# Optimization experiments

Hardware: AMD Instinct MI355X
Metric: run time of the kernel (lower is better)

## Reference

```python
import jax, jax.numpy as jnp
import numpy as np

NC, NG, NP = 8192, 4096, 140
FD, D, L = 512, 256, 2
E_OBS, E_COEXP, E_PPI, E_SYM = 300000, 200000, 10000, 20000
EPS = 1e-5


def layer_norm(x, g, b):
    mu = jnp.mean(x, -1, keepdims=True)
    v = jnp.mean((x - mu) ** 2, -1, keepdims=True)
    return (x - mu) * jax.lax.rsqrt(v + EPS) * g + b


def sage(h_src, h_dst, src, dst, w, Ws, Wn, b, n_dst):
    # DGL SAGEConv (mean aggregator, edge-weighted): mean over incoming
    # weighted messages, then fc_self(h_dst) + fc_neigh(neigh) + bias.
    m = h_src[src] * w[:, None]                                  # [E, D]
    neigh = jax.ops.segment_sum(m, dst, num_segments=n_dst)      # [n_dst, D]
    deg = jax.ops.segment_sum(jnp.ones_like(w), dst, num_segments=n_dst)
    neigh = neigh / jnp.maximum(deg, 1.0)[:, None]
    return h_dst @ Ws + neigh @ Wn + b


def setup_inputs() -> dict:
    key = jax.random.key(0)
    ks = iter(jax.random.split(key, 64))
    def n(*s):
        return jax.random.normal(next(ks), s, jnp.float32) * 0.02
    def u(e):
        return jax.random.uniform(next(ks), (e,), jnp.float32)
    def ri(e, hi):
        return jax.random.randint(next(ks), (e,), 0, hi, jnp.int32)
    return dict(
        cell_feat=jax.random.normal(next(ks), (NC, FD), jnp.float32),
        gene_feat=jax.random.normal(next(ks), (NG, FD), jnp.float32),
        pro_idx=jnp.arange(NP, dtype=jnp.int32),
        obs_src=ri(E_OBS, NG), obs_dst=ri(E_OBS, NC), obs_w=u(E_OBS),
        rev_obs_src=ri(E_OBS, NC), rev_obs_dst=ri(E_OBS, NG), rev_obs_w=u(E_OBS),
        symbol_src=ri(E_SYM, NG), symbol_dst=ri(E_SYM, NP), symbol_w=u(E_SYM),
        rev_symbol_src=ri(E_SYM, NP), rev_symbol_dst=ri(E_SYM, NG), rev_symbol_w=u(E_SYM),
        coexp_src=ri(E_COEXP, NG), coexp_dst=ri(E_COEXP, NG), coexp_w=u(E_COEXP),
        ppi_src=ri(E_PPI, NP), ppi_dst=ri(E_PPI, NP), ppi_w=u(E_PPI),
        W_emb_cell=n(FD, D), b_emb_cell=jnp.zeros((D,), jnp.float32),
        W_emb_gene=n(FD, D), b_emb_gene=jnp.zeros((D,), jnp.float32),
        emb_pro=n(NP, D),
        W_mlpcell=n(L, D, D), b_mlpcell=jnp.zeros((L, D), jnp.float32),
        W_sage_self=n(L, 6, D, D), W_sage_neigh=n(L, 6, D, D),
        b_sage=jnp.zeros((L, 6, D), jnp.float32),
        ln1_g=jnp.ones((L, 3, D), jnp.float32), ln1_b=jnp.zeros((L, 3, D), jnp.float32),
        ln2_g=jnp.ones((L, 3, D), jnp.float32), ln2_b=jnp.zeros((L, 3, D), jnp.float32),
        W_last=n(3 * D, NP), b_last=jnp.zeros((NP,), jnp.float32),
    )


def reference(cell_feat, gene_feat, pro_idx,
              obs_src, obs_dst, obs_w,
              rev_obs_src, rev_obs_dst, rev_obs_w,
              symbol_src, symbol_dst, symbol_w,
              rev_symbol_src, rev_symbol_dst, rev_symbol_w,
              coexp_src, coexp_dst, coexp_w,
              ppi_src, ppi_dst, ppi_w,
              W_emb_cell, b_emb_cell, W_emb_gene, b_emb_gene, emb_pro,
              W_mlpcell, b_mlpcell, W_sage_self, W_sage_neigh, b_sage,
              ln1_g, ln1_b, ln2_g, ln2_b, W_last, b_last):
    act = jax.nn.selu
    hc = cell_feat @ W_emb_cell + b_emb_cell      # emb_cell
    hg = gene_feat @ W_emb_gene + b_emb_gene      # emb_gene
    hp = emb_pro[pro_idx]                         # nn.Embedding path
    nc, ng, npn = hc.shape[0], hg.shape[0], hp.shape[0]
    hist = [hc]
    for l in range(W_mlpcell.shape[0]):
        Ws, Wn, bs = W_sage_self[l], W_sage_neigh[l], b_sage[l]
        hmlp = layer_norm(act(hc @ W_mlpcell[l] + b_mlpcell[l]), ln1_g[l, 2], ln1_b[l, 2])
        # HeteroGraphConv(SAGE) over edges_sub = [obs, rev_obs, symbol, rev_symbol] (stack)
        s_obs = sage(hg, hc, obs_src, obs_dst, obs_w, Ws[0], Wn[0], bs[0], nc)
        s_robs = sage(hc, hg, rev_obs_src, rev_obs_dst, rev_obs_w, Ws[1], Wn[1], bs[1], ng)
        s_sym = sage(hg, hp, symbol_src, symbol_dst, symbol_w, Ws[2], Wn[2], bs[2], npn)
        s_rsym = sage(hp, hg, rev_symbol_src, rev_symbol_dst, rev_symbol_w, Ws[3], Wn[3], bs[3], ng)
        # homogeneous subgraph convs: gene_sage on coexp, pro_sage on ppi
        h_gg = layer_norm(act(sage(hg, hg, coexp_src, coexp_dst, coexp_w, Ws[4], Wn[4], bs[4], ng)), ln1_g[l, 0], ln1_b[l, 0])
        h_pp = layer_norm(act(sage(hp, hp, ppi_src, ppi_dst, ppi_w, Ws[5], Wn[5], bs[5], npn)), ln1_g[l, 1], ln1_b[l, 1])
        # norm each stacked relation output, then agg='sum' over the stack dim
        hgen = layer_norm(act(s_robs), ln1_g[l, 0], ln1_b[l, 0]) + layer_norm(act(s_rsym), ln1_g[l, 0], ln1_b[l, 0]) + h_gg
        hpro = layer_norm(act(s_sym), ln1_g[l, 1], ln1_b[l, 1]) + h_pp
        hcel = layer_norm(act(s_obs), ln1_g[l, 2], ln1_b[l, 2]) + hmlp
        hg = layer_norm(act(hgen), ln2_g[l, 0], ln2_b[l, 0])
        hp = layer_norm(act(hpro), ln2_g[l, 1], ln2_b[l, 1])
        hc = layer_norm(act(hcel), ln2_g[l, 2], ln2_b[l, 2])
        hist.append(hc)
    # mlp_last over concat of per-layer cell reps (sum(dims[1:-1]) -> dims[-1])
    return jnp.concatenate(hist, -1) @ W_last + b_last
```

## Files before the change

kernel.cpp:

```cpp
#include <hip/hip_runtime.h>

typedef unsigned short ushort_t;
typedef unsigned int uint_t;

typedef ushort_t ushortx8 __attribute__((ext_vector_type(8)));
typedef ushort_t ushortx4 __attribute__((ext_vector_type(4)));
typedef __bf16 bf16x8 __attribute__((ext_vector_type(8)));
typedef float f32x4 __attribute__((ext_vector_type(4)));

#define NCC 8192
#define NGG 4096
#define NPP 140
#define LDS_STR 88
#define CEPB 16384

__device__ __forceinline__ float bf2f(ushort_t u) {
    uint_t i = ((uint_t)u) << 16;
    float f;
    __builtin_memcpy(&f, &i, 4);
    return f;
}
__device__ __forceinline__ ushort_t f2bf(float f) {
    uint_t i;
    __builtin_memcpy(&i, &f, 4);
    uint_t r = (i + 0x7FFFu + ((i >> 16) & 1u)) >> 16;
    return (ushort_t)r;
}
__device__ __forceinline__ float scrub(float x) {
    return __builtin_isfinite(x) ? x : 0.f;
}
__device__ __forceinline__ float selu_f(float x) {
    return x > 0.f ? 1.0507009873554805f * x : 1.7580993408473766f * expm1f(x);
}
__device__ __forceinline__ float wsum64(float x) {
    for (int o = 32; o; o >>= 1) x += __shfl_xor(x, o, 64);
    return x;
}

__global__ __launch_bounds__(256) void sc_zero1(int* __restrict__ a, int na) {
    int i = blockIdx.x * 256 + threadIdx.x;
    if (i < na) a[i] = 0;
}

struct CountJob {
    const int* dst;
    const int* src;
    const float* w;
    uint_t* pw;
    ushort_t* rank;
    int E;
    int nbins;
    int* deg;
    int bstart;
};
struct CountBatch {
    CountJob j[6];
};
struct TrJob {
    const float* src;
    ushort_t* dst;
    int K, N, nx, nxy;
    int bstart;
};
struct TrBatch {
    TrJob j[6];
};
struct FillJob {
    const int* dst;
    const uint_t* pw;
    const ushort_t* rank;
    int E;
    const int* offs;
    uint_t* ep;
    int bstart;
};
struct FillBatch {
    FillJob j[6];
};
struct GemmJob {
    const void* A1;
    int lda1, K1, af1;
    const ushort_t* Bt1;
    const ushort_t* A2;
    int K2;
    const ushort_t* Bt2;
    const float* bias;
    ushort_t* C;
    int ldc, M;
    int mstart;
};
struct GemmBatch {
    GemmJob j[7];
};

struct CountArgs {
    CountBatch cb;
    int bsC;
    const float* cf;
    ushort_t* cf16;
    int nbC;
    int nbCvt;
    const float* gf;
    ushort_t* gf16;
    TrBatch tb;
    int bsT;
    const float* emb;
    const int* pidx;
    ushort_t* hp;
    int nEmb;
};
__global__ __launch_bounds__(1024) void sc_count(CountArgs ca) {
    __shared__ int hist[NCC];
    int bx = blockIdx.x;
    const int tid = threadIdx.x;
    if (bx >= ca.bsC) {
        bx -= ca.bsC;
        if (bx < ca.nbCvt) {
            const float* src;
            ushort_t* dst;
            if (bx < ca.nbC) {
                src = ca.cf;
                dst = ca.cf16;
            } else {
                bx -= ca.nbC;
                src = ca.gf;
                dst = ca.gf16;
            }
            size_t i = ((size_t)bx * 1024 + tid) * 8;
            float4 f0 = *(const float4*)(src + i);
            float4 f1 = *(const float4*)(src + i + 4);
            ushortx8 v;
            v[0] = f2bf(f0.x);
            v[1] = f2bf(f0.y);
            v[2] = f2bf(f0.z);
            v[3] = f2bf(f0.w);
            v[4] = f2bf(f1.x);
            v[5] = f2bf(f1.y);
            v[6] = f2bf(f1.z);
            v[7] = f2bf(f1.w);
            *(ushortx8*)(dst + i) = v;
            return;
        }
        bx -= ca.nbCvt;
        if (bx < ca.bsT) {
            ushort_t* tt = (ushort_t*)hist;
            int r = 0;
#pragma unroll
            for (int i = 1; i < 6; ++i) r = (bx >= ca.tb.j[i].bstart) ? i : r;
            const TrJob& J = ca.tb.j[r];
            int local = bx - J.bstart;
            int b = local / J.nxy, rem = local % J.nxy;
            int n0 = (rem % J.nx) * 32, k0 = (rem / J.nx) * 32;
            const float* s = J.src + (size_t)b * J.K * J.N;
            ushort_t* d = J.dst + (size_t)b * J.K * J.N;
            int x = tid & 31, y = tid >> 5;
            {
                int k = k0 + y, n = n0 + x;
                tt[y * 33 + x] = (k < J.K && n < J.N) ? f2bf(s[(size_t)k * J.N + n]) : (ushort_t)0;
            }
            __syncthreads();
            {
                int n = n0 + y, k = k0 + x;
                if (n < J.N && k < J.K) d[(size_t)n * J.K + k] = tt[x * 33 + y];
            }
            return;
        }
        bx -= ca.bsT;
        int i = bx * 1024 + tid;
        if (i < ca.nEmb) {
            int r = i >> 8, c = i & 255;
            int j = ca.pidx[r];
            j = (uint_t)j < (uint_t)NPP ? j : 0;
            ca.hp[i] = f2bf(ca.emb[(size_t)j * 256 + c]);
        }
        return;
    }
    int r = 0;
#pragma unroll
    for (int i = 1; i < 6; ++i) r = (bx >= ca.cb.j[i].bstart) ? i : r;
    const CountJob& J = ca.cb.j[r];
    const int nb = J.nbins;
    for (int b = tid; b < nb; b += 1024) hist[b] = 0;
    __syncthreads();
    const int e0 = (bx - J.bstart) * CEPB;
    ushort_t lrk[16];
#pragma unroll
    for (int u = 0; u < 16; ++u) {
        int e = e0 + u * 1024 + tid;
        if (e < J.E) {
            int d = J.dst[e];
            lrk[u] = (ushort_t)atomicAdd(&hist[d], 1);
            J.pw[e] = ((uint_t)f2bf(J.w[e]) << 16) | (uint_t)J.src[e];
        }
    }
    __syncthreads();
    for (int b = tid; b < nb; b += 1024) {
        int c = hist[b];
        if (c > 0) hist[b] = atomicAdd(&J.deg[b], c);
    }
    __syncthreads();
#pragma unroll
    for (int u = 0; u < 16; ++u) {
        int e = e0 + u * 1024 + tid;
        if (e < J.E) {
            int d = J.dst[e];
            J.rank[e] = (ushort_t)(hist[d] + (int)lrk[u]);
        }
    }
}

__global__ __launch_bounds__(1024) void sc_csr_scan6(const int* __restrict__ deg_base,
                                                     int* __restrict__ offs_base) {
    const int ndst[6] = {NCC, NGG, NPP, NGG, NGG, NPP};
    const int dstart[6] = {0, NCC, NCC + NGG, NCC + NGG + NPP, NCC + 2 * NGG + NPP,
                           NCC + 3 * NGG + NPP};
    const int ostart[6] = {0, NCC + 1, NCC + NGG + 2, NCC + NGG + NPP + 3,
                           NCC + 2 * NGG + NPP + 4, NCC + 3 * NGG + NPP + 5};
    int r = blockIdx.x;
    const int* deg = deg_base + dstart[r];
    int* offs = offs_base + ostart[r];
    int n = ndst[r];
    __shared__ int wsum[16];
    __shared__ int carry;
    int tid = threadIdx.x, wave = tid >> 6, lane = tid & 63;
    if (tid == 0) carry = 0;
    __syncthreads();
    for (int base = 0; base < n; base += 1024) {
        int i = base + tid;
        int v = (i < n) ? deg[i] : 0;
        int x = v;
#pragma unroll
        for (int o = 1; o < 64; o <<= 1) {
            int tv = __shfl_up(x, o, 64);
            if (lane >= o) x += tv;
        }
        if (lane == 63) wsum[wave] = x;
        __syncthreads();
        if (tid == 0) {
            int acc = 0;
#pragma unroll
            for (int k = 0; k < 16; ++k) {
                int tv = wsum[k];
                wsum[k] = acc;
                acc += tv;
            }
        }
        __syncthreads();
        int incl = x + wsum[wave];
        int cr = carry;
        if (i < n) offs[i] = cr + incl - v;
        __syncthreads();
        if (tid == 1023) carry = cr + incl;
        __syncthreads();
    }
    if (tid == 0) offs[n] = carry;
}

__device__ __forceinline__ void gemm_body(const GemmBatch& gbat, int mbx, int n0, ushort_t* As,
                                          ushort_t* Bs) {
    int r = 0;
#pragma unroll
    for (int i = 1; i < 7; ++i) r = (mbx >= gbat.j[i].mstart) ? i : r;
    const void* JA1 = gbat.j[r].A1;
    const int lda1 = gbat.j[r].lda1, K1j = gbat.j[r].K1, af1 = gbat.j[r].af1;
    const ushort_t* JBt1 = gbat.j[r].Bt1;
    const ushort_t* JA2 = gbat.j[r].A2;
    const int K2j = gbat.j[r].K2;
    const ushort_t* JBt2 = gbat.j[r].Bt2;
    const float* bias = gbat.j[r].bias;
    ushort_t* C = gbat.j[r].C;
    const int ldc = gbat.j[r].ldc, M = gbat.j[r].M;
    const int tid = threadIdx.x;
    const int wave = tid >> 6, lane = tid & 63;
    const int lr = lane & 15, lq = lane >> 4;
    const int m0 = (mbx - gbat.j[r].mstart) * 128;
    f32x4 acc[2][4] = {};
    for (int pass = 0; pass < 2; ++pass) {
        const void* A = pass ? (const void*)JA2 : JA1;
        const ushort_t* Bt = pass ? JBt2 : JBt1;
        const int K = pass ? K2j : K1j;
        const int lda = pass ? 256 : lda1;
        const int af = pass ? 0 : af1;
        if (K == 0 || A == nullptr) continue;
        for (int k0 = 0; k0 < K; k0 += 64) {
            __syncthreads();
#pragma unroll
            for (int i = 0; i < 4; ++i) {
                int g = tid + i * 256;
                int rr = g >> 3, c = (g & 7) * 8;
                ushortx8 v = {0, 0, 0, 0, 0, 0, 0, 0};
                int gm = m0 + rr;
                if (gm < M) {
                    if (af) {
                        const float* Af = (const float*)A;
                        float4 f0 = *(const float4*)(Af + (size_t)gm * lda + k0 + c);
                        float4 f1 = *(const float4*)(Af + (size_t)gm * lda + k0 + c + 4);
                        v[0] = f2bf(f0.x);
                        v[1] = f2bf(f0.y);
                        v[2] = f2bf(f0.z);
                        v[3] = f2bf(f0.w);
                        v[4] = f2bf(f1.x);
                        v[5] = f2bf(f1.y);
                        v[6] = f2bf(f1.z);
                        v[7] = f2bf(f1.w);
                    } else {
                        v = *(const ushortx8*)((const ushort_t*)A + (size_t)gm * lda + k0 + c);
                    }
                }
                *(ushortx8*)(&As[rr * LDS_STR + c]) = v;
            }
#pragma unroll
            for (int i = 0; i < 2; ++i) {
                int g = tid + i * 256;
                int rr = g >> 3, c = (g & 7) * 8;
                int gn = n0 + rr;
                ushortx8 v = *(const ushortx8*)(Bt + (size_t)gn * K + k0 + c);
                *(ushortx8*)(&Bs[rr * LDS_STR + c]) = v;
            }
            __syncthreads();
#pragma unroll
            for (int kk = 0; kk < 64; kk += 32) {
                bf16x8 a0 = __builtin_bit_cast(
                    bf16x8, *(const ushortx8*)(&As[(wave * 32 + lr) * LDS_STR + kk + lq * 8]));
                bf16x8 a1 = __builtin_bit_cast(
                    bf16x8,
                    *(const ushortx8*)(&As[(wave * 32 + 16 + lr) * LDS_STR + kk + lq * 8]));
                bf16x8 b0 = __builtin_bit_cast(
                    bf16x8, *(const ushortx8*)(&Bs[(lr)*LDS_STR + kk + lq * 8]));
                bf16x8 b1 = __builtin_bit_cast(
                    bf16x8, *(const ushortx8*)(&Bs[(16 + lr) * LDS_STR + kk + lq * 8]));
                bf16x8 b2 = __builtin_bit_cast(
                    bf16x8, *(const ushortx8*)(&Bs[(32 + lr) * LDS_STR + kk + lq * 8]));
                bf16x8 b3 = __builtin_bit_cast(
                    bf16x8, *(const ushortx8*)(&Bs[(48 + lr) * LDS_STR + kk + lq * 8]));
                acc[0][0] = __builtin_amdgcn_mfma_f32_16x16x32_bf16(a0, b0, acc[0][0], 0, 0, 0);
                acc[0][1] = __builtin_amdgcn_mfma_f32_16x16x32_bf16(a0, b1, acc[0][1], 0, 0, 0);
                acc[0][2] = __builtin_amdgcn_mfma_f32_16x16x32_bf16(a0, b2, acc[0][2], 0, 0, 0);
                acc[0][3] = __builtin_amdgcn_mfma_f32_16x16x32_bf16(a0, b3, acc[0][3], 0, 0, 0);
                acc[1][0] = __builtin_amdgcn_mfma_f32_16x16x32_bf16(a1, b0, acc[1][0], 0, 0, 0);
                acc[1][1] = __builtin_amdgcn_mfma_f32_16x16x32_bf16(a1, b1, acc[1][1], 0, 0, 0);
                acc[1][2] = __builtin_amdgcn_mfma_f32_16x16x32_bf16(a1, b2, acc[1][2], 0, 0, 0);
                acc[1][3] = __builtin_amdgcn_mfma_f32_16x16x32_bf16(a1, b3, acc[1][3], 0, 0, 0);
            }
        }
    }
#pragma unroll
    for (int mt = 0; mt < 2; ++mt)
#pragma unroll
        for (int nt = 0; nt < 4; ++nt) {
            int col = n0 + nt * 16 + lr;
            float bb = bias[col];
#pragma unroll
            for (int v = 0; v < 4; ++v) {
                int row = m0 + wave * 32 + mt * 16 + lq * 4 + v;
                if (row >= M) continue;
                C[(size_t)row * ldc + col] = f2bf(scrub(acc[mt][nt][v] + bb));
            }
        }
}

__global__ __launch_bounds__(256) void sc_gemm_batch(GemmBatch gbat) {
    __shared__ __align__(16) ushort_t As[128 * LDS_STR];
    __shared__ __align__(16) ushort_t Bs[64 * LDS_STR];
    gemm_body(gbat, blockIdx.x, blockIdx.y * 64, As, Bs);
}

struct Emb64Job {
    const ushort_t* A;
    const ushort_t* Bt;
    const float* bias;
    ushort_t* C;
    int ldc;
    ushort_t* C2;
    int mstart;
};
struct FillGemmArgs {
    Emb64Job ej[2];
    int gemmBlocks;
    FillBatch fb;
};
__global__ __launch_bounds__(256) void sc_fill_gemm(FillGemmArgs fg) {
    __shared__ __align__(16) ushort_t As[64 * LDS_STR];
    __shared__ __align__(16) ushort_t Bs[64 * LDS_STR];
    int bx = blockIdx.x;
    if (bx >= fg.gemmBlocks) {
        bx -= fg.gemmBlocks;
        int r = 0;
#pragma unroll
        for (int i = 1; i < 6; ++i) r = (bx >= fg.fb.j[i].bstart) ? i : r;
        const FillJob& J = fg.fb.j[r];
        int e = (bx - J.bstart) * 256 + threadIdx.x;
        if (e < J.E) {
            int d = J.dst[e];
            J.ep[J.offs[d] + (int)J.rank[e]] = J.pw[e];
        }
        return;
    }
    const int mb = bx >> 2, n0 = (bx & 3) * 64;
    const int r = (mb >= fg.ej[1].mstart) ? 1 : 0;
    const Emb64Job& J = fg.ej[r];
    const int m0 = (mb - J.mstart) * 64;
    const ushort_t* A = J.A;
    const ushort_t* Bt = J.Bt;
    const int tid = threadIdx.x;
    const int wave = tid >> 6, lane = tid & 63;
    const int lr = lane & 15, lq = lane >> 4;
    f32x4 acc[4] = {};
    for (int k0 = 0; k0 < 512; k0 += 64) {
        __syncthreads();
#pragma unroll
        for (int i = 0; i < 2; ++i) {
            int g = tid + i * 256;
            int rr = g >> 3, c = (g & 7) * 8;
            *(ushortx8*)(&As[rr * LDS_STR + c]) =
                *(const ushortx8*)(A + (size_t)(m0 + rr) * 512 + k0 + c);
            *(ushortx8*)(&Bs[rr * LDS_STR + c]) =
                *(const ushortx8*)(Bt + (size_t)(n0 + rr) * 512 + k0 + c);
        }
        __syncthreads();
#pragma unroll
        for (int kk = 0; kk < 64; kk += 32) {
            bf16x8 a = __builtin_bit_cast(
                bf16x8, *(const ushortx8*)(&As[(wave * 16 + lr) * LDS_STR + kk + lq * 8]));
            bf16x8 b0 =
                __builtin_bit_cast(bf16x8, *(const ushortx8*)(&Bs[(lr)*LDS_STR + kk + lq * 8]));
            bf16x8 b1 = __builtin_bit_cast(
                bf16x8, *(const ushortx8*)(&Bs[(16 + lr) * LDS_STR + kk + lq * 8]));
            bf16x8 b2 = __builtin_bit_cast(
                bf16x8, *(const ushortx8*)(&Bs[(32 + lr) * LDS_STR + kk + lq * 8]));
            bf16x8 b3 = __builtin_bit_cast(
                bf16x8, *(const ushortx8*)(&Bs[(48 + lr) * LDS_STR + kk + lq * 8]));
            acc[0] = __builtin_amdgcn_mfma_f32_16x16x32_bf16(a, b0, acc[0], 0, 0, 0);
            acc[1] = __builtin_amdgcn_mfma_f32_16x16x32_bf16(a, b1, acc[1], 0, 0, 0);
            acc[2] = __builtin_amdgcn_mfma_f32_16x16x32_bf16(a, b2, acc[2], 0, 0, 0);
            acc[3] = __builtin_amdgcn_mfma_f32_16x16x32_bf16(a, b3, acc[3], 0, 0, 0);
        }
    }
#pragma unroll
    for (int nt = 0; nt < 4; ++nt) {
        int col = n0 + nt * 16 + lr;
        float bb = J.bias[col];
#pragma unroll
        for (int v = 0; v < 4; ++v) {
            int row = m0 + wave * 16 + lq * 4 + v;
            ushort_t val = f2bf(scrub(acc[nt][v] + bb));
            J.C[(size_t)row * J.ldc + col] = val;
            if (J.C2) J.C2[(size_t)row * 256 + col] = val;
// ... 38 lines not shown
                *(ushortx8*)(&As[rr * LDS_STR + c]) =
                    *(const ushortx8*)(ga.mA + (size_t)(m0 + rr) * 768 + k0 + c);
                *(ushortx8*)(&Bs[rr * LDS_STR + c]) =
                    *(const ushortx8*)(ga.mBt + (size_t)(n0 + rr) * 256 + k0 + c);
            }
            __syncthreads();
#pragma unroll
            for (int kk = 0; kk < 64; kk += 32) {
                bf16x8 a = __builtin_bit_cast(
                    bf16x8, *(const ushortx8*)(&As[(wave * 16 + lr) * LDS_STR + kk + lq * 8]));
                bf16x8 b0 = __builtin_bit_cast(
                    bf16x8, *(const ushortx8*)(&Bs[(lr)*LDS_STR + kk + lq * 8]));
                bf16x8 b1 = __builtin_bit_cast(
                    bf16x8, *(const ushortx8*)(&Bs[(16 + lr) * LDS_STR + kk + lq * 8]));
                bf16x8 b2 = __builtin_bit_cast(
                    bf16x8, *(const ushortx8*)(&Bs[(32 + lr) * LDS_STR + kk + lq * 8]));
                bf16x8 b3 = __builtin_bit_cast(
                    bf16x8, *(const ushortx8*)(&Bs[(48 + lr) * LDS_STR + kk + lq * 8]));
                acc[0] = __builtin_amdgcn_mfma_f32_16x16x32_bf16(a, b0, acc[0], 0, 0, 0);
                acc[1] = __builtin_amdgcn_mfma_f32_16x16x32_bf16(a, b1, acc[1], 0, 0, 0);
                acc[2] = __builtin_amdgcn_mfma_f32_16x16x32_bf16(a, b2, acc[2], 0, 0, 0);
                acc[3] = __builtin_amdgcn_mfma_f32_16x16x32_bf16(a, b3, acc[3], 0, 0, 0);
            }
        }
#pragma unroll
        for (int nt = 0; nt < 4; ++nt) {
            int col = n0 + nt * 16 + lr;
            float bb = ga.mbias[col];
#pragma unroll
            for (int v = 0; v < 4; ++v) {
                int row = m0 + wave * 16 + lq * 4 + v;
                ga.mC[(size_t)row * 256 + col] = f2bf(scrub(acc[nt][v] + bb));
            }
        }
        return;
    }
    bx -= ga.gemmBlocks;
    int grow = bx * 4 + (tid >> 6);
    if (grow >= ga.total_rows) return;
    int r = 0;
#pragma unroll
    for (int i = 1; i < 6; ++i) r = (grow >= ga.j[i].row_start) ? i : r;
    r = __builtin_amdgcn_readfirstlane(r);
    const char* hsrc = (const char*)ga.j[r].hsrc;
    const uint_t row_bytes = (uint_t)(ga.j[r].src_ld * 2);
    const uint_t src_n = (uint_t)ga.j[r].src_n;
    const int* offs = ga.j[r].offs;
    const uint_t* ep = ga.j[r].ep;
    ushort_t* out = ga.j[r].out;
    int row = grow - ga.j[r].row_start;
    int lane = tid & 63;
    int cb = lane * 8;
    int s0 = offs[row], s1 = offs[row + 1];
    float a0 = 0.f, a1 = 0.f, a2 = 0.f, a3 = 0.f;
    for (int base = s0; base < s1; base += 64) {
        int e = base + lane;
        uint_t myp = (e < s1) ? ep[e] : 0u;
        int cnt = s1 - base;
        cnt = cnt < 64 ? cnt : 64;
        int cnt16 = (cnt + 15) & ~15;
        for (int jj = 0; jj < cnt16; jj += 16) {
#pragma unroll
            for (int u = 0; u < 16; ++u) {
                uint_t pw = (uint_t)__builtin_amdgcn_readlane((int)myp, jj + u);
                uint_t s = pw & 0xFFFFu;
                s = s < src_n ? s : 0u;
                float w = bf2f((ushort_t)(pw >> 16));
                const uint2 v = *(const uint2*)(hsrc + (size_t)(s * row_bytes) + cb);
                uint_t x0 = v.x << 16, x1 = v.x & 0xFFFF0000u;
                uint_t x2 = v.y << 16, x3 = v.y & 0xFFFF0000u;
                a0 = fmaf(w, __builtin_bit_cast(float, x0), a0);
                a1 = fmaf(w, __builtin_bit_cast(float, x1), a1);
                a2 = fmaf(w, __builtin_bit_cast(float, x2), a2);
                a3 = fmaf(w, __builtin_bit_cast(float, x3), a3);
            }
        }
    }
    float inv = 1.f / fmaxf((float)(s1 - s0), 1.f);
    ushort_t* o = out + (size_t)row * 256 + lane * 4;
    o[0] = f2bf(scrub(a0 * inv));
    o[1] = f2bf(scrub(a1 * inv));
    o[2] = f2bf(scrub(a2 * inv));
    o[3] = f2bf(scrub(a3 * inv));
}

__global__ __launch_bounds__(256) void sc_gemm(const ushort_t* __restrict__ A1, int lda1,
                                               const ushort_t* __restrict__ Bt1, int K1,
                                               const float* __restrict__ bias,
                                               float* __restrict__ Cf, int ldc, int M, int N) {
    __shared__ __align__(16) ushort_t As[128 * LDS_STR];
    __shared__ __align__(16) ushort_t Bs[64 * LDS_STR];
    const int tid = threadIdx.x;
    const int wave = tid >> 6, lane = tid & 63;
    const int lr = lane & 15, lq = lane >> 4;
    const int m0 = blockIdx.x * 128, n0 = blockIdx.y * 64;
    f32x4 acc[2][4] = {};
    for (int k0 = 0; k0 < K1; k0 += 64) {
        __syncthreads();
#pragma unroll
        for (int i = 0; i < 4; ++i) {
            int g = tid + i * 256;
            int r = g >> 3, c = (g & 7) * 8;
            ushortx8 v = {0, 0, 0, 0, 0, 0, 0, 0};
            int gm = m0 + r;
            if (gm < M) v = *(const ushortx8*)(A1 + (size_t)gm * lda1 + k0 + c);
            *(ushortx8*)(&As[r * LDS_STR + c]) = v;
        }
#pragma unroll
        for (int i = 0; i < 2; ++i) {
            int g = tid + i * 256;
            int r = g >> 3, c = (g & 7) * 8;
            ushortx8 v = {0, 0, 0, 0, 0, 0, 0, 0};
            int gn = n0 + r;
            if (gn < N) v = *(const ushortx8*)(Bt1 + (size_t)gn * K1 + k0 + c);
            *(ushortx8*)(&Bs[r * LDS_STR + c]) = v;
        }
        __syncthreads();
#pragma unroll
        for (int kk = 0; kk < 64; kk += 32) {
            bf16x8 a0 = __builtin_bit_cast(
                bf16x8, *(const ushortx8*)(&As[(wave * 32 + lr) * LDS_STR + kk + lq * 8]));
            bf16x8 a1 = __builtin_bit_cast(
                bf16x8, *(const ushortx8*)(&As[(wave * 32 + 16 + lr) * LDS_STR + kk + lq * 8]));
            bf16x8 b0 =
                __builtin_bit_cast(bf16x8, *(const ushortx8*)(&Bs[(lr)*LDS_STR + kk + lq * 8]));
            bf16x8 b1 = __builtin_bit_cast(
                bf16x8, *(const ushortx8*)(&Bs[(16 + lr) * LDS_STR + kk + lq * 8]));
            bf16x8 b2 = __builtin_bit_cast(
                bf16x8, *(const ushortx8*)(&Bs[(32 + lr) * LDS_STR + kk + lq * 8]));
            bf16x8 b3 = __builtin_bit_cast(
                bf16x8, *(const ushortx8*)(&Bs[(48 + lr) * LDS_STR + kk + lq * 8]));
            acc[0][0] = __builtin_amdgcn_mfma_f32_16x16x32_bf16(a0, b0, acc[0][0], 0, 0, 0);
            acc[0][1] = __builtin_amdgcn_mfma_f32_16x16x32_bf16(a0, b1, acc[0][1], 0, 0, 0);
            acc[0][2] = __builtin_amdgcn_mfma_f32_16x16x32_bf16(a0, b2, acc[0][2], 0, 0, 0);
            acc[0][3] = __builtin_amdgcn_mfma_f32_16x16x32_bf16(a0, b3, acc[0][3], 0, 0, 0);
            acc[1][0] = __builtin_amdgcn_mfma_f32_16x16x32_bf16(a1, b0, acc[1][0], 0, 0, 0);
            acc[1][1] = __builtin_amdgcn_mfma_f32_16x16x32_bf16(a1, b1, acc[1][1], 0, 0, 0);
            acc[1][2] = __builtin_amdgcn_mfma_f32_16x16x32_bf16(a1, b2, acc[1][2], 0, 0, 0);
            acc[1][3] = __builtin_amdgcn_mfma_f32_16x16x32_bf16(a1, b3, acc[1][3], 0, 0, 0);
        }
    }
#pragma unroll
    for (int mt = 0; mt < 2; ++mt)
#pragma unroll
        for (int nt = 0; nt < 4; ++nt) {
            int col = n0 + nt * 16 + lr;
            if (col >= N) continue;
            float bb = bias ? bias[col] : 0.f;
#pragma unroll
            for (int v = 0; v < 4; ++v) {
                int row = m0 + wave * 32 + mt * 16 + lq * 4 + v;
                if (row >= M) continue;
                Cf[(size_t)row * ldc + col] = scrub(acc[mt][nt][v] + bb);
            }
        }
}

struct LnJob {
    const ushort_t *sA, *sB, *sC;
    const float *g1, *b1, *g2, *b2;
    ushort_t* out;
    int out_ld;
    ushort_t* out2;
    int row_start;
};
struct LnBatch {
// ... 83 lines not shown
    const float* b_sage = (const float*)d_in[30];
    const float* ln1_g = (const float*)d_in[31];
    const float* ln1_b = (const float*)d_in[32];
    const float* ln2_g = (const float*)d_in[33];
    const float* ln2_b = (const float*)d_in[34];
    const float* W_last = (const float*)d_in[35];
    const float* b_last = (const float*)d_in[36];

    const int E_obs = in_sizes[3], E_sym = in_sizes[9], E_coexp = in_sizes[15],
              E_ppi = in_sizes[18];
    const int Er[6] = {E_obs, E_obs, E_sym, E_sym, E_coexp, E_ppi};
    const int Nd[6] = {NCC, NGG, NPP, NGG, NGG, NPP};

    char* p = (char*)d_ws;
    auto carve = [&](size_t bytes) -> char* {
        char* r = p;
        p += ((bytes + 255) & ~(size_t)255);
        return r;
    };
    ushort_t* hist = (ushort_t*)carve((size_t)NCC * 768 * 2);
    ushort_t* hg = (ushort_t*)carve((size_t)NGG * 256 * 2);
    ushort_t* hp = (ushort_t*)carve((size_t)NPP * 256 * 2);
    ushort_t* n_obs = (ushort_t*)carve((size_t)NCC * 256 * 2);
    ushort_t* n_robs = (ushort_t*)carve((size_t)NGG * 256 * 2);
    ushort_t* n_sym = (ushort_t*)carve((size_t)NPP * 256 * 2);
    ushort_t* n_rsym = (ushort_t*)carve((size_t)NGG * 256 * 2);
    ushort_t* n_coexp = (ushort_t*)carve((size_t)NGG * 256 * 2);
    ushort_t* n_ppi = (ushort_t*)carve((size_t)NPP * 256 * 2);
    ushort_t* s_obs = (ushort_t*)carve((size_t)NCC * 256 * 2);
    ushort_t* s_robs = (ushort_t*)carve((size_t)NGG * 256 * 2);
    ushort_t* s_sym = (ushort_t*)carve((size_t)NPP * 256 * 2);
    ushort_t* s_rsym = (ushort_t*)carve((size_t)NGG * 256 * 2);
    ushort_t* s_coexp = (ushort_t*)carve((size_t)NGG * 256 * 2);
    ushort_t* s_ppi = (ushort_t*)carve((size_t)NPP * 256 * 2);
    ushort_t* s_mlp = (ushort_t*)carve((size_t)NCC * 256 * 2);
    ushort_t* Wt_emb_cell = (ushort_t*)carve((size_t)512 * 256 * 2);
    ushort_t* Wt_emb_gene = (ushort_t*)carve((size_t)512 * 256 * 2);
    ushort_t* Wt_mlp = (ushort_t*)carve((size_t)2 * 256 * 256 * 2);
    ushort_t* Wt_self = (ushort_t*)carve((size_t)12 * 256 * 256 * 2);
    ushort_t* Wt_neigh = (ushort_t*)carve((size_t)12 * 256 * 256 * 2);
    ushort_t* Wt_last = (ushort_t*)carve((size_t)140 * 768 * 2);
    const int NDTOT = NCC + 3 * NGG + 2 * NPP;
    int* deg_all = (int*)carve((size_t)NDTOT * 4);
    int* offs_all = (int*)carve((size_t)(NDTOT + 6) * 4);
    const int ETOT = 2 * E_obs + 2 * E_sym + E_coexp + E_ppi;
    uint_t* pw_all = (uint_t*)carve((size_t)ETOT * 4);
    ushort_t* rank_all = (ushort_t*)carve((size_t)ETOT * 2);
    uint_t* ep_all = (uint_t*)carve((size_t)ETOT * 4);
    ushort_t* hc_cmp = (ushort_t*)carve((size_t)NCC * 256 * 2);
    ushort_t* cf16 = s_obs;
    ushort_t* gf16 = s_coexp;
    (void)ws_size;
    (void)n_in;
    (void)out_size;

    const int dS[6] = {0, NCC, NCC + NGG, NCC + NGG + NPP, NCC + 2 * NGG + NPP,
                       NCC + 3 * NGG + NPP};
    const int oS[6] = {0, NCC + 1, NCC + NGG + 2, NCC + NGG + NPP + 3, NCC + 2 * NGG + NPP + 4,
                       NCC + 3 * NGG + NPP + 5};
    int eS[6];
    eS[0] = 0;
    eS[1] = eS[0] + E_obs;
    eS[2] = eS[1] + E_obs;
    eS[3] = eS[2] + E_sym;
    eS[4] = eS[3] + E_sym;
    eS[5] = eS[4] + E_coexp;

    sc_zero1<<<cdivi(NDTOT, 256), 256, 0, stream>>>(deg_all, NDTOT);
    {
        CountArgs ca;
        int bs = 0;
        for (int r = 0; r < 6; ++r) {
            ca.cb.j[r] = {edge_dst[r], edge_src[r], edge_w[r], pw_all + eS[r], rank_all + eS[r],
                          Er[r],       Nd[r],       deg_all + dS[r], bs};
            bs += cdivi(Er[r], CEPB);
        }
        ca.bsC = bs;
        ca.cf = cell_feat;
        ca.cf16 = cf16;
        ca.nbC = (NCC * 512) / 8192;
        ca.gf = gene_feat;
        ca.gf16 = gf16;
        int nbG = (NGG * 512) / 8192;
        ca.nbCvt = ca.nbC + nbG;
        int bt = 0;
        auto add = [&](int idx, const float* s, ushort_t* d, int B, int K, int N) {
            int nx = cdivi(N, 32), ny = cdivi(K, 32);
            ca.tb.j[idx] = {s, d, K, N, nx, nx * ny, bt};
            bt += B * nx * ny;
        };
        add(0, W_emb_cell, Wt_emb_cell, 1, 512, 256);
        add(1, W_emb_gene, Wt_emb_gene, 1, 512, 256);
        add(2, W_mlpcell, Wt_mlp, 2, 256, 256);
        add(3, W_sage_self, Wt_self, 12, 256, 256);
        add(4, W_sage_neigh, Wt_neigh, 12, 256, 256);
        add(5, W_last, Wt_last, 1, 768, 140);
        ca.bsT = bt;
        ca.emb = emb_pro;
        ca.pidx = pro_idx;
        ca.hp = hp;
        ca.nEmb = NPP * 256;
        int bsE = cdivi(NPP * 256, 1024);
        sc_count<<<bs + ca.nbCvt + bt + bsE, 1024, 0, stream>>>(ca);
    }
    sc_csr_scan6<<<6, 1024, 0, stream>>>(deg_all, offs_all);
    {
        FillGemmArgs fg;
        fg.ej[0] = {cf16, Wt_emb_cell, b_emb_cell, hist, 768, hc_cmp, 0};
        fg.ej[1] = {gf16, Wt_emb_gene, b_emb_gene, hg, 256, nullptr, NCC / 64};
        fg.gemmBlocks = (NCC / 64 + NGG / 64) * 4;
        int bs = 0;
        for (int r = 0; r < 6; ++r) {
            fg.fb.j[r] = {edge_dst[r], pw_all + eS[r], rank_all + eS[r], Er[r], offs_all + oS[r],
                          ep_all + eS[r], bs};
            bs += cdivi(Er[r], 256);
        }
        sc_fill_gemm<<<fg.gemmBlocks + bs, 256, 0, stream>>>(fg);
    }

    for (int l = 0; l < 2; ++l) {
        const ushort_t* hc_l = hist + l * 256;
        {
            GatherMlpArgs ga;
            const ushort_t* hs[6] = {hg, hc_cmp, hg, hp, hg, hp};
            const int sn[6] = {NGG, NCC, NGG, NPP, NGG, NPP};
            ushort_t* outs[6] = {n_obs, n_robs, n_sym, n_rsym, n_coexp, n_ppi};
            int rs = 0;
            for (int r = 0; r < 6; ++r) {
                ga.j[r] = {hs[r], 256, sn[r], offs_all + oS[r], ep_all + eS[r], outs[r], rs};
                rs += Nd[r];
            }
            ga.gemmBlocks = (NCC / 64) * 4;
            ga.mA = hc_l;
            ga.mBt = Wt_mlp + (size_t)l * 65536;
            ga.mbias = b_mlpcell + l * 256;
            ga.mC = s_mlp;
            ga.total_rows = rs;
            sc_gather_mlp<<<ga.gemmBlocks + cdivi(rs, 4), 256, 0, stream>>>(ga);
        }
        {
            const size_t WSZ = 65536;
            GemmBatch gbat;
            const ushort_t* dstf[6] = {hc_l, hg, hp, hg, hg, hp};
            const int dld[6] = {768, 256, 256, 256, 256, 256};
            const ushort_t* nb[6] = {n_obs, n_robs, n_sym, n_rsym, n_coexp, n_ppi};
            ushort_t* so[6] = {s_obs, s_robs, s_sym, s_rsym, s_coexp, s_ppi};
            int ms = 0;
            for (int r = 0; r < 6; ++r) {
                gbat.j[r] = {dstf[r],
                             dld[r],
                             256,
                             0,
                             Wt_self + (size_t)(l * 6 + r) * WSZ,
                             nb[r],
                             256,
                             Wt_neigh + (size_t)(l * 6 + r) * WSZ,
                             b_sage + (l * 6 + r) * 256,
                             so[r],
                             256,
                             Nd[r],
                             ms};
                ms += cdivi(Nd[r], 128);
            }
            gbat.j[6] = gbat.j[5];
            gbat.j[6].mstart = 0x7FFFFFFF;
            sc_gemm_batch<<<dim3(ms, 4), 256, 0, stream>>>(gbat);
        }
        {
            LnBatch lb;
            lb.j[0] = {s_robs, s_rsym, s_coexp, ln1_g + (l * 3 + 0) * 256,
                       ln1_b + (l * 3 + 0) * 256, ln2_g + (l * 3 + 0) * 256,
                       ln2_b + (l * 3 + 0) * 256, hg, 256, nullptr, 0};
            lb.j[1] = {s_sym, s_ppi, nullptr, ln1_g + (l * 3 + 1) * 256,
                       ln1_b + (l * 3 + 1) * 256, ln2_g + (l * 3 + 1) * 256,
                       ln2_b + (l * 3 + 1) * 256, hp, 256, nullptr, NGG};
            lb.j[2] = {s_obs, s_mlp, nullptr, ln1_g + (l * 3 + 2) * 256,
                       ln1_b + (l * 3 + 2) * 256, ln2_g + (l * 3 + 2) * 256,
                       ln2_b + (l * 3 + 2) * 256, hist + (l + 1) * 256, 768,
                       (l == 0) ? hc_cmp : nullptr, NGG + NPP};
            int rs = NGG + NPP + NCC;
            sc_fuse_ln_all<<<cdivi(rs, 4), 256, 0, stream>>>(lb, rs);
        }
    }

    sc_gemm<<<dim3(64, 3), 256, 0, stream>>>(hist, 768, Wt_last, 768, b_last, (float*)d_out, 140,
                                             NCC, 140);
}
```

Measured before the change: 381.2 us.

## Replicate count histograms, fold transpose into scan kernel, use 64-row SAGE GEMM tiles

The edge-count kernel now keeps several replicated LDS histograms when the bin count is small, which spreads atomic contention on hot bins, and it assigns ranks per replica. The weight transpose and protein-embedding work move out of the count kernel into the CSR scan kernel, so the count kernel's 1024-thread blocks no longer carry that extra work. The batched SAGE GEMM switches from 128-row to 64-row tiles, which doubles the block count for better CU occupancy at the cost of less B-tile reuse. The change adds a second launch path and more LDS zeroing work per count block.

```diff
diff --git a/kernel.cpp b/kernel.cpp
--- a/kernel.cpp
+++ b/kernel.cpp
@@ -77,21 +77,6 @@
 struct FillBatch {
     FillJob j[6];
 };
-struct GemmJob {
-    const void* A1;
-    int lda1, K1, af1;
-    const ushort_t* Bt1;
-    const ushort_t* A2;
-    int K2;
-    const ushort_t* Bt2;
-    const float* bias;
-    ushort_t* C;
-    int ldc, M;
-    int mstart;
-};
-struct GemmBatch {
-    GemmJob j[7];
-};
 
 struct CountArgs {
     CountBatch cb;
@@ -99,9 +84,95 @@
     const float* cf;
     ushort_t* cf16;
     int nbC;
-    int nbCvt;
     const float* gf;
     ushort_t* gf16;
+};
+__global__ __launch_bounds__(1024) void sc_count(CountArgs ca) {
+    __shared__ int hist[NCC];
+    int bx = blockIdx.x;
+    const int tid = threadIdx.x;
+    if (bx >= ca.bsC) {
+        bx -= ca.bsC;
+        const float* src;
+        ushort_t* dst;
+        if (bx < ca.nbC) {
+            src = ca.cf;
+            dst = ca.cf16;
+        } else {
+            bx -= ca.nbC;
+            src = ca.gf;
+            dst = ca.gf16;
+        }
+        size_t i = ((size_t)bx * 1024 + tid) * 8;
+        float4 f0 = *(const float4*)(src + i);
+        float4 f1 = *(const float4*)(src + i + 4);
+        ushortx8 v;
+        v[0] = f2bf(f0.x);
+        v[1] = f2bf(f0.y);
+        v[2] = f2bf(f0.z);
+        v[3] = f2bf(f0.w);
+        v[4] = f2bf(f1.x);
+        v[5] = f2bf(f1.y);
+        v[6] = f2bf(f1.z);
+        v[7] = f2bf(f1.w);
+        *(ushortx8*)(dst + i) = v;
+        return;
+    }
+    int r = 0;
+#pragma unroll
+    for (int i = 1; i < 6; ++i) r = (bx >= ca.cb.j[i].bstart) ? i : r;
+    const CountJob& J = ca.cb.j[r];
+    const int nb = J.nbins;
+    const int rep = nb <= 1024 ? 8 : (nb <= 4096 ? 2 : 1);
+    const int qoff = (tid & (rep - 1)) * nb;
+    const int tot_bins = nb * rep;
+    for (int b = tid; b < tot_bins; b += 1024) hist[b] = 0;
+    __syncthreads();
+    const int e0 = (bx - J.bstart) * CEPB;
+    ushort_t lrk[16];
+#pragma unroll
+    for (int u = 0; u < 16; ++u) {
+        int e = e0 + u * 1024 + tid;
+        if (e < J.E) {
+            int d = J.dst[e];
+            lrk[u] = (ushort_t)atomicAdd(&hist[qoff + d], 1);
+            J.pw[e] = ((uint_t)f2bf(J.w[e]) << 16) | (uint_t)J.src[e];
+        }
+    }
+    __syncthreads();
+    for (int b = tid; b < nb; b += 1024) {
+        int c[8];
+        int tot = 0;
+#pragma unroll
+        for (int q = 0; q < 8; ++q) {
+            c[q] = (q < rep) ? hist[q * nb + b] : 0;
+            tot += c[q];
+        }
+        if (tot > 0) {
+            int run = atomicAdd(&J.deg[b], tot);
+#pragma unroll
+            for (int q = 0; q < 8; ++q) {
+                if (q < rep) {
+                    hist[q * nb + b] = run;
+                    run += c[q];
+                }
+            }
+        }
+    }
+    __syncthreads();
+#pragma unroll
+    for (int u = 0; u < 16; ++u) {
+        int e = e0 + u * 1024 + tid;
+        if (e < J.E) {
+            int d = J.dst[e];
+            J.rank[e] = (ushort_t)(hist[qoff + d] + (int)lrk[u]);
+        }
+    }
+}
+
+struct ScanPrepArgs {
+    const int* deg_base;
+    int* offs_base;
     TrBatch tb;
     int bsT;
     const float* emb;
@@ -109,45 +180,19 @@
     ushort_t* hp;
     int nEmb;
 };
-__global__ __launch_bounds__(1024) void sc_count(CountArgs ca) {
-    __shared__ int hist[NCC];
+__global__ __launch_bounds__(1024) void sc_scan_prep(ScanPrepArgs sa) {
+    __shared__ int wsum[16];
+    __shared__ int carry;
+    __shared__ ushort_t tt[32 * 33];
     int bx = blockIdx.x;
     const int tid = threadIdx.x;
-    if (bx >= ca.bsC) {
-        bx -= ca.bsC;
-        if (bx < ca.nbCvt) {
-            const float* src;
-            ushort_t* dst;
-            if (bx < ca.nbC) {
-                src = ca.cf;
-                dst = ca.cf16;
-            } else {
-                bx -= ca.nbC;
-                src = ca.gf;
-                dst = ca.gf16;
-            }
-            size_t i = ((size_t)bx * 1024 + tid) * 8;
-            float4 f0 = *(const float4*)(src + i);
-            float4 f1 = *(const float4*)(src + i + 4);
-            ushortx8 v;
-            v[0] = f2bf(f0.x);
-            v[1] = f2bf(f0.y);
-            v[2] = f2bf(f0.z);
-            v[3] = f2bf(f0.w);
-            v[4] = f2bf(f1.x);
-            v[5] = f2bf(f1.y);
-            v[6] = f2bf(f1.z);
-            v[7] = f2bf(f1.w);
-            *(ushortx8*)(dst + i) = v;
-            return;
-        }
-        bx -= ca.nbCvt;
-        if (bx < ca.bsT) {
-            ushort_t* tt = (ushort_t*)hist;
+    if (bx >= 6) {
+        bx -= 6;
+        if (bx < sa.bsT) {
             int r = 0;
 #pragma unroll
-            for (int i = 1; i < 6; ++i) r = (bx >= ca.tb.j[i].bstart) ? i : r;
-            const TrJob& J = ca.tb.j[r];
+            for (int i = 1; i < 6; ++i) r = (bx >= sa.tb.j[i].bstart) ? i : r;
+            const TrJob& J = sa.tb.j[r];
             int local = bx - J.bstart;
             int b = local / J.nxy, rem = local % J.nxy;
             int n0 = (rem % J.nx) * 32, k0 = (rem / J.nx) * 32;
@@ -156,7 +201,8 @@
             int x = tid & 31, y = tid >> 5;
             {
                 int k = k0 + y, n = n0 + x;
-                tt[y * 33 + x] = (k < J.K && n < J.N) ? f2bf(s[(size_t)k * J.N + n]) : (ushort_t)0;
+                tt[y * 33 + x] =
+                    (k < J.K && n < J.N) ? f2bf(s[(size_t)k * J.N + n]) : (ushort_t)0;
             }
             __syncthreads();
             {
@@ -165,64 +211,26 @@
             }
             return;
         }
-        bx -= ca.bsT;
+        bx -= sa.bsT;
         int i = bx * 1024 + tid;
-        if (i < ca.nEmb) {
+        if (i < sa.nEmb) {
             int r = i >> 8, c = i & 255;
-            int j = ca.pidx[r];
+            int j = sa.pidx[r];
             j = (uint_t)j < (uint_t)NPP ? j : 0;
-            ca.hp[i] = f2bf(ca.emb[(size_t)j * 256 + c]);
+            sa.hp[i] = f2bf(sa.emb[(size_t)j * 256 + c]);
         }
         return;
     }
-    int r = 0;
-#pragma unroll
-    for (int i = 1; i < 6; ++i) r = (bx >= ca.cb.j[i].bstart) ? i : r;
-    const CountJob& J = ca.cb.j[r];
-    const int nb = J.nbins;
-    for (int b = tid; b < nb; b += 1024) hist[b] = 0;
-    __syncthreads();
-    const int e0 = (bx - J.bstart) * CEPB;
-    ushort_t lrk[16];
-#pragma unroll
-    for (int u = 0; u < 16; ++u) {
-        int e = e0 + u * 1024 + tid;
-        if (e < J.E) {
-            int d = J.dst[e];
-            lrk[u] = (ushort_t)atomicAdd(&hist[d], 1);
-            J.pw[e] = ((uint_t)f2bf(J.w[e]) << 16) | (uint_t)J.src[e];
-        }
-    }
-    __syncthreads();
-    for (int b = tid; b < nb; b += 1024) {
-        int c = hist[b];
-        if (c > 0) hist[b] = atomicAdd(&J.deg[b], c);
-    }
-    __syncthreads();
-#pragma unroll
-    for (int u = 0; u < 16; ++u) {
-        int e = e0 + u * 1024 + tid;
-        if (e < J.E) {
-            int d = J.dst[e];
-            J.rank[e] = (ushort_t)(hist[d] + (int)lrk[u]);
-        }
-    }
-}
-
-__global__ __launch_bounds__(1024) void sc_csr_scan6(const int* __restrict__ deg_base,
-                                                     int* __restrict__ offs_base) {
     const int ndst[6] = {NCC, NGG, NPP, NGG, NGG, NPP};
     const int dstart[6] = {0, NCC, NCC + NGG, NCC + NGG + NPP, NCC + 2 * NGG + NPP,
                            NCC + 3 * NGG + NPP};
     const int ostart[6] = {0, NCC + 1, NCC + NGG + 2, NCC + NGG + NPP + 3,
                            NCC + 2 * NGG + NPP + 4, NCC + 3 * NGG + NPP + 5};
-    int r = blockIdx.x;
-    const int* deg = deg_base + dstart[r];
-    int* offs = offs_base + ostart[r];
+    int r = bx;
+    const int* deg = sa.deg_base + dstart[r];
+    int* offs = sa.offs_base + ostart[r];
     int n = ndst[r];
-    __shared__ int wsum[16];
-    __shared__ int carry;
-    int tid = threadIdx.x, wave = tid >> 6, lane = tid & 63;
+    int wave = tid >> 6, lane = tid & 63;
     if (tid == 0) carry = 0;
     __syncthreads();
     for (int base = 0; base < n; base += 1024) {
@@ -254,115 +262,6 @@
         __syncthreads();
     }
     if (tid == 0) offs[n] = carry;
-}
-
-__device__ __forceinline__ void gemm_body(const GemmBatch& gbat, int mbx, int n0, ushort_t* As,
-                                          ushort_t* Bs) {
-    int r = 0;
-#pragma unroll
-    for (int i = 1; i < 7; ++i) r = (mbx >= gbat.j[i].mstart) ? i : r;
-    const void* JA1 = gbat.j[r].A1;
-    const int lda1 = gbat.j[r].lda1, K1j = gbat.j[r].K1, af1 = gbat.j[r].af1;
-    const ushort_t* JBt1 = gbat.j[r].Bt1;
-    const ushort_t* JA2 = gbat.j[r].A2;
-    const int K2j = gbat.j[r].K2;
-    const ushort_t* JBt2 = gbat.j[r].Bt2;
-    const float* bias = gbat.j[r].bias;
-    ushort_t* C = gbat.j[r].C;
-    const int ldc = gbat.j[r].ldc, M = gbat.j[r].M;
-    const int tid = threadIdx.x;
-    const int wave = tid >> 6, lane = tid & 63;
-    const int lr = lane & 15, lq = lane >> 4;
-    const int m0 = (mbx - gbat.j[r].mstart) * 128;
-    f32x4 acc[2][4] = {};
-    for (int pass = 0; pass < 2; ++pass) {
-        const void* A = pass ? (const void*)JA2 : JA1;
-        const ushort_t* Bt = pass ? JBt2 : JBt1;
-        const int K = pass ? K2j : K1j;
-        const int lda = pass ? 256 : lda1;
-        const int af = pass ? 0 : af1;
-        if (K == 0 || A == nullptr) continue;
-        for (int k0 = 0; k0 < K; k0 += 64) {
-            __syncthreads();
-#pragma unroll
-            for (int i = 0; i < 4; ++i) {
-                int g = tid + i * 256;
-                int rr = g >> 3, c = (g & 7) * 8;
-                ushortx8 v = {0, 0, 0, 0, 0, 0, 0, 0};
-                int gm = m0 + rr;
-                if (gm < M) {
-                    if (af) {
-                        const float* Af = (const float*)A;
-                        float4 f0 = *(const float4*)(Af + (size_t)gm * lda + k0 + c);
-                        float4 f1 = *(const float4*)(Af + (size_t)gm * lda + k0 + c + 4);
-                        v[0] = f2bf(f0.x);
-                        v[1] = f2bf(f0.y);
-                        v[2] = f2bf(f0.z);
-                        v[3] = f2bf(f0.w);
-                        v[4] = f2bf(f1.x);
-                        v[5] = f2bf(f1.y);
-                        v[6] = f2bf(f1.z);
-                        v[7] = f2bf(f1.w);
-                    } else {
-                        v = *(const ushortx8*)((const ushort_t*)A + (size_t)gm * lda + k0 + c);
-                    }
-                }
-                *(ushortx8*)(&As[rr * LDS_STR + c]) = v;
-            }
-#pragma unroll
-            for (int i = 0; i < 2; ++i) {
-                int g = tid + i * 256;
-                int rr = g >> 3, c = (g & 7) * 8;
-                int gn = n0 + rr;
-                ushortx8 v = *(const ushortx8*)(Bt + (size_t)gn * K + k0 + c);
-                *(ushortx8*)(&Bs[rr * LDS_STR + c]) = v;
-            }
-            __syncthreads();
-#pragma unroll
-            for (int kk = 0; kk < 64; kk += 32) {
-                bf16x8 a0 = __builtin_bit_cast(
-                    bf16x8, *(const ushortx8*)(&As[(wave * 32 + lr) * LDS_STR + kk + lq * 8]));
-                bf16x8 a1 = __builtin_bit_cast(
-                    bf16x8,
-                    *(const ushortx8*)(&As[(wave * 32 + 16 + lr) * LDS_STR + kk + lq * 8]));
-                bf16x8 b0 = __builtin_bit_cast(
-                    bf16x8, *(const ushortx8*)(&Bs[(lr)*LDS_STR + kk + lq * 8]));
-                bf16x8 b1 = __builtin_bit_cast(
-                    bf16x8, *(const ushortx8*)(&Bs[(16 + lr) * LDS_STR + kk + lq * 8]));
-                bf16x8 b2 = __builtin_bit_cast(
-                    bf16x8, *(const ushortx8*)(&Bs[(32 + lr) * LDS_STR + kk + lq * 8]));
-                bf16x8 b3 = __builtin_bit_cast(
-                    bf16x8, *(const ushortx8*)(&Bs[(48 + lr) * LDS_STR + kk + lq * 8]));
-                acc[0][0] = __builtin_amdgcn_mfma_f32_16x16x32_bf16(a0, b0, acc[0][0], 0, 0, 0);
-                acc[0][1] = __builtin_amdgcn_mfma_f32_16x16x32_bf16(a0, b1, acc[0][1], 0, 0, 0);
-                acc[0][2] = __builtin_amdgcn_mfma_f32_16x16x32_bf16(a0, b2, acc[0][2], 0, 0, 0);
-                acc[0][3] = __builtin_amdgcn_mfma_f32_16x16x32_bf16(a0, b3, acc[0][3], 0, 0, 0);
-                acc[1][0] = __builtin_amdgcn_mfma_f32_16x16x32_bf16(a1, b0, acc[1][0], 0, 0, 0);
-                acc[1][1] = __builtin_amdgcn_mfma_f32_16x16x32_bf16(a1, b1, acc[1][1], 0, 0, 0);
-                acc[1][2] = __builtin_amdgcn_mfma_f32_16x16x32_bf16(a1, b2, acc[1][2], 0, 0, 0);
-                acc[1][3] = __builtin_amdgcn_mfma_f32_16x16x32_bf16(a1, b3, acc[1][3], 0, 0, 0);
-            }
-        }
-    }
-#pragma unroll
-    for (int mt = 0; mt < 2; ++mt)
-#pragma unroll
-        for (int nt = 0; nt < 4; ++nt) {
-            int col = n0 + nt * 16 + lr;
-            float bb = bias[col];
-#pragma unroll
-            for (int v = 0; v < 4; ++v) {
-                int row = m0 + wave * 32 + mt * 16 + lq * 4 + v;
-                if (row >= M) continue;
-                C[(size_t)row * ldc + col] = f2bf(scrub(acc[mt][nt][v] + bb));
-            }
-        }
-}
-
-__global__ __launch_bounds__(256) void sc_gemm_batch(GemmBatch gbat) {
-    __shared__ __align__(16) ushort_t As[128 * LDS_STR];
-    __shared__ __align__(16) ushort_t Bs[64 * LDS_STR];
-    gemm_body(gbat, blockIdx.x, blockIdx.y * 64, As, Bs);
 }
 
 struct Emb64Job {
@@ -567,6 +466,84 @@
     o[1] = f2bf(scrub(a1 * inv));
     o[2] = f2bf(scrub(a2 * inv));
     o[3] = f2bf(scrub(a3 * inv));
+}
+
+struct Sage64Job {
+    const ushort_t* A1;
+    int lda1;
+    const ushort_t* Bt1;
+    const ushort_t* A2;
+    const ushort_t* Bt2;
+    const float* bias;
+    ushort_t* C;
+    int M;
+    int mstart;
+};
+struct Sage64Batch {
+    Sage64Job j[6];
+};
+__global__ __launch_bounds__(256) void sc_gemm_batch64(Sage64Batch gb) {
+    __shared__ __align__(16) ushort_t As[64 * LDS_STR];
+    __shared__ __align__(16) ushort_t Bs[64 * LDS_STR];
+    const int mbx = blockIdx.x, n0 = blockIdx.y * 64;
+    int r = 0;
+#pragma unroll
+    for (int i = 1; i < 6; ++i) r = (mbx >= gb.j[i].mstart) ? i : r;
+    const Sage64Job& J = gb.j[r];
+    const int m0 = (mbx - J.mstart) * 64;
+    const int M = J.M;
+    const int tid = threadIdx.x;
+    const int wave = tid >> 6, lane = tid & 63;
+    const int lr = lane & 15, lq = lane >> 4;
+    f32x4 acc[4] = {};
+    for (int pass = 0; pass < 2; ++pass) {
+        const ushort_t* A = pass ? J.A2 : J.A1;
+        const int lda = pass ? 256 : J.lda1;
+        const ushort_t* Bt = pass ? J.Bt2 : J.Bt1;
+        for (int k0 = 0; k0 < 256; k0 += 64) {
+            __syncthreads();
+#pragma unroll
+            for (int i = 0; i < 2; ++i) {
+                int g = tid + i * 256;
+                int rr = g >> 3, c = (g & 7) * 8;
+                int gm = m0 + rr;
+                ushortx8 v = {0, 0, 0, 0, 0, 0, 0, 0};
+                if (gm < M) v = *(const ushortx8*)(A + (size_t)gm * lda + k0 + c);
+                *(ushortx8*)(&As[rr * LDS_STR + c]) = v;
+                *(ushortx8*)(&Bs[rr * LDS_STR + c]) =
+                    *(const ushortx8*)(Bt + (size_t)(n0 + rr) * 256 + k0 + c);
+            }
+            __syncthreads();
+#pragma unroll
+            for (int kk = 0; kk < 64; kk += 32) {
+                bf16x8 a = __builtin_bit_cast(
+                    bf16x8, *(const ushortx8*)(&As[(wave * 16 + lr) * LDS_STR + kk + lq * 8]));
+                bf16x8 b0 = __builtin_bit_cast(
+                    bf16x8, *(const ushortx8*)(&Bs[(lr)*LDS_STR + kk + lq * 8]));
+                bf16x8 b1 = __builtin_bit_cast(
+                    bf16x8, *(const ushortx8*)(&Bs[(16 + lr) * LDS_STR + kk + lq * 8]));
+                bf16x8 b2 = __builtin_bit_cast(
+                    bf16x8, *(const ushortx8*)(&Bs[(32 + lr) * LDS_STR + kk + lq * 8]));
+                bf16x8 b3 = __builtin_bit_cast(
+                    bf16x8, *(const ushortx8*)(&Bs[(48 + lr) * LDS_STR + kk + lq * 8]));
+                acc[0] = __builtin_amdgcn_mfma_f32_16x16x32_bf16(a, b0, acc[0], 0, 0, 0);
+                acc[1] = __builtin_amdgcn_mfma_f32_16x16x32_bf16(a, b1, acc[1], 0, 0, 0);
+                acc[2] = __builtin_amdgcn_mfma_f32_16x16x32_bf16(a, b2, acc[2], 0, 0, 0);
+                acc[3] = __builtin_amdgcn_mfma_f32_16x16x32_bf16(a, b3, acc[3], 0, 0, 0);
+            }
+        }
+    }
+#pragma unroll
+    for (int nt = 0; nt < 4; ++nt) {
+        int col = n0 + nt * 16 + lr;
+        float bb = J.bias[col];
+#pragma unroll
+        for (int v = 0; v < 4; ++v) {
+            int row = m0 + wave * 16 + lq * 4 + v;
+            if (row >= M) continue;
+            J.C[(size_t)row * 256 + col] = f2bf(scrub(acc[nt][v] + bb));
+        }
+    }
 }
 
 __global__ __launch_bounds__(256) void sc_gemm(const ushort_t* __restrict__ A1, int lda1,
@@ -816,11 +793,16 @@
         ca.gf = gene_feat;
         ca.gf16 = gf16;
         int nbG = (NGG * 512) / 8192;
-        ca.nbCvt = ca.nbC + nbG;
+        sc_count<<<bs + ca.nbC + nbG, 1024, 0, stream>>>(ca);
+    }
+    {
+        ScanPrepArgs sa;
+        sa.deg_base = deg_all;
+        sa.offs_base = offs_all;
         int bt = 0;
         auto add = [&](int idx, const float* s, ushort_t* d, int B, int K, int N) {
             int nx = cdivi(N, 32), ny = cdivi(K, 32);
-            ca.tb.j[idx] = {s, d, K, N, nx, nx * ny, bt};
+            sa.tb.j[idx] = {s, d, K, N, nx, nx * ny, bt};
             bt += B * nx * ny;
         };
         add(0, W_emb_cell, Wt_emb_cell, 1, 512, 256);
@@ -829,15 +811,14 @@
         add(3, W_sage_self, Wt_self, 12, 256, 256);
         add(4, W_sage_neigh, Wt_neigh, 12, 256, 256);
         add(5, W_last, Wt_last, 1, 768, 140);
-        ca.bsT = bt;
-        ca.emb = emb_pro;
-        ca.pidx = pro_idx;
-        ca.hp = hp;
-        ca.nEmb = NPP * 256;
+        sa.bsT = bt;
+        sa.emb = emb_pro;
+        sa.pidx = pro_idx;
+        sa.hp = hp;
+        sa.nEmb = NPP * 256;
         int bsE = cdivi(NPP * 256, 1024);
-        sc_count<<<bs + ca.nbCvt + bt + bsE, 1024, 0, stream>>>(ca);
-    }
-    sc_csr_scan6<<<6, 1024, 0, stream>>>(deg_all, offs_all);
+        sc_scan_prep<<<6 + bt + bsE, 1024, 0, stream>>>(sa);
+    }
     {
         FillGemmArgs fg;
         fg.ej[0] = {cf16, Wt_emb_cell, b_emb_cell, hist, 768, hc_cmp, 0};
@@ -874,31 +855,25 @@
         }
         {
             const size_t WSZ = 65536;
-            GemmBatch gbat;
+            Sage64Batch gb;
             const ushort_t* dstf[6] = {hc_l, hg, hp, hg, hg, hp};
             const int dld[6] = {768, 256, 256, 256, 256, 256};
             const ushort_t* nb[6] = {n_obs, n_robs, n_sym, n_rsym, n_coexp, n_ppi};
             ushort_t* so[6] = {s_obs, s_robs, s_sym, s_rsym, s_coexp, s_ppi};
             int ms = 0;
             for (int r = 0; r < 6; ++r) {
-                gbat.j[r] = {dstf[r],
-                             dld[r],
-                             256,
-                             0,
-                             Wt_self + (size_t)(l * 6 + r) * WSZ,
-                             nb[r],
-                             256,
-                             Wt_neigh + (size_t)(l * 6 + r) * WSZ,
-                             b_sage + (l * 6 + r) * 256,
-                             so[r],
-                             256,
-                             Nd[r],
-                             ms};
-                ms += cdivi(Nd[r], 128);
-            }
-            gbat.j[6] = gbat.j[5];
-            gbat.j[6].mstart = 0x7FFFFFFF;
-            sc_gemm_batch<<<dim3(ms, 4), 256, 0, stream>>>(gbat);
+                gb.j[r] = {dstf[r],
+                           dld[r],
+                           Wt_self + (size_t)(l * 6 + r) * WSZ,
+                           nb[r],
+                           Wt_neigh + (size_t)(l * 6 + r) * WSZ,
+                           b_sage + (l * 6 + r) * 256,
+                           so[r],
+                           Nd[r],
+                           ms};
+                ms += cdivi(Nd[r], 64);
+            }
+            sc_gemm_batch64<<<dim3(ms, 4), 256, 0, stream>>>(gb);
         }
         {
             LnBatch lb;
```

Result: faster. 370.5 us (-2.8%).
